# Optimization experiments

Hardware: AMD Instinct MI355X
Metric: run time of the kernel (lower is better)

## Reference

```python
import jax, jax.numpy as jnp
import numpy as np

B, T, D = 4096, 200, 128
K_SHORT = 5


def setup_inputs() -> dict:
    key = jax.random.key(0)
    ks = jax.random.split(key, 8)
    hist_items = jax.random.normal(ks[0], (B, T, D), dtype=jnp.float32)
    hist_mask = jax.random.randint(ks[1], (B, T), 0, 2).astype(bool)
    hist_mask = hist_mask.at[:, 0].set(True)  # avoid fully-masked rows
    hist_age_hours = jax.random.uniform(ks[2], (B, T), dtype=jnp.float32) * 168.0
    hist_popularity = jax.random.uniform(ks[3], (B, T), dtype=jnp.float32)
    s = 1.0 / float(np.sqrt(D))
    Wq = jax.random.normal(ks[4], (D, D), dtype=jnp.float32) * s
    Wk = jax.random.normal(ks[5], (D, D), dtype=jnp.float32) * s
    Wv = jax.random.normal(ks[6], (D, D), dtype=jnp.float32) * s
    gate_w = jax.random.normal(ks[7], (1, 2), dtype=jnp.float32) * 0.5
    gate_b = jnp.zeros((1,), dtype=jnp.float32)
    ln_gamma = jnp.ones((D,), dtype=jnp.float32)
    ln_beta = jnp.zeros((D,), dtype=jnp.float32)
    decay_alpha = jnp.asarray(0.05, dtype=jnp.float32)
    return {"hist_items": hist_items, "hist_mask": hist_mask,
            "hist_age_hours": hist_age_hours, "hist_popularity": hist_popularity,
            "Wq": Wq, "Wk": Wk, "Wv": Wv, "gate_w": gate_w, "gate_b": gate_b,
            "ln_gamma": ln_gamma, "ln_beta": ln_beta, "decay_alpha": decay_alpha}


def reference(hist_items, hist_mask, hist_age_hours, hist_popularity,
              Wq, Wk, Wv, gate_w, gate_b, ln_gamma, ln_beta, decay_alpha):
    dt = hist_items.dtype
    maskf = hist_mask.astype(dt)  # (B,T)
    # learnable time-decay bias
    alpha = jax.nn.softplus(decay_alpha) + 1e-6
    decay = jnp.exp(-alpha * hist_age_hours) * maskf  # (B,T)
    # masked mean of history as the single query
    mean_hist = (hist_items * maskf[..., None]).sum(1) / (maskf.sum(1, keepdims=True) + 1e-6)  # (B,D)
    q = mean_hist @ Wq.T                                # (B,D)
    k = jnp.einsum('btd,ed->bte', hist_items, Wk)       # (B,T,D)
    v = jnp.einsum('btd,ed->bte', hist_items, Wv)       # (B,T,D)
    scale = 1.0 / float(np.sqrt(hist_items.shape[-1]))
    scores = jnp.einsum('bd,btd->bt', q, k) * scale + jnp.log(decay + 1e-12)
    scores = jnp.where(hist_mask, scores, -jnp.inf)
    attn = jax.nn.softmax(scores, axis=-1)              # (B,T)
    long_term = jnp.einsum('bt,btd->bd', attn, v)       # (B,D)
    # vectorized last-K window: positions [cnt-K, cnt)
    cnt = jnp.maximum(hist_mask.sum(1), 1)              # (B,) int
    K = min(K_SHORT, hist_items.shape[1])
    ar = jnp.arange(hist_items.shape[1])[None, :]       # (1,T)
    lastk = (ar >= (cnt[:, None] - K)) & (ar < cnt[:, None])  # (B,T) bool
    lk = lastk.astype(dt)
    denom = jnp.maximum(lk.sum(1, keepdims=True), 1.0)  # (B,1)
    short_term = (hist_items * lk[..., None]).sum(1) / denom  # (B,D)
    mean_pop = (hist_popularity * lk).sum(1) / denom[:, 0]
    mean_rec = (hist_age_hours * lk).sum(1) / denom[:, 0]
    ctx = jnp.stack([mean_pop, mean_rec], axis=-1)      # (B,2)
    g = jax.nn.sigmoid(ctx @ gate_w.T + gate_b)         # (B,1)
    user = g * short_term + (1.0 - g) * long_term       # (B,D)
    # LayerNorm (eps=1e-5, biased variance, matching torch)
    mu = user.mean(-1, keepdims=True)
    var = user.var(-1, keepdims=True)
    return (user - mu) / jnp.sqrt(var + 1e-5) * ln_gamma + ln_beta
```

## Files before the change

kernel.cpp:

```cpp
#include <hip/hip_runtime.h>

#define BB 4096
#define TT 200
#define DD 128
#define KSHORT 5

__device__ __forceinline__ unsigned short f2bf(float x) {
  union { float f; unsigned u; } c; c.f = x;
  unsigned r = c.u + 0x7fffu + ((c.u >> 16) & 1u);
  return (unsigned short)(r >> 16);
}
__device__ __forceinline__ float bf2f(unsigned short h) {
  union { unsigned u; float f; } c; c.u = ((unsigned)h) << 16;
  return c.f;
}

__global__ void detect_mask_kernel(const unsigned* __restrict__ m, int* __restrict__ flag) {
  unsigned bad = 0;
  for (int i = threadIdx.x; i < 1024; i += 64) bad |= (m[i] > 1u) ? 1u : 0u;
  unsigned long long bl = __ballot(bad != 0u);
  if (threadIdx.x == 0) *flag = (bl != 0ULL) ? 1 : 0;
}

__global__ void precompute_A_kernel(const float* __restrict__ Wq,
                                    const float* __restrict__ Wk,
                                    float* __restrict__ A) {
  const int d = blockIdx.x, dp = threadIdx.x;
  float acc = 0.f;
#pragma unroll 8
  for (int e = 0; e < DD; ++e) acc += Wk[e * DD + d] * Wq[e * DD + dp];
  A[d * DD + dp] = acc;
}

__global__ __launch_bounds__(512, 4) void arig_main_kernel(
    const float* __restrict__ items, const void* __restrict__ maskp,
    const float* __restrict__ age, const float* __restrict__ pop,
    const float* __restrict__ Wv, const float* __restrict__ gate_w,
    const float* __restrict__ gate_b, const float* __restrict__ gamma,
    const float* __restrict__ beta, const float* __restrict__ alpha_in,
    const float* __restrict__ A, const int* __restrict__ flagp,
    float* __restrict__ out) {
  __shared__ unsigned short s_items[TT * DD];
  __shared__ float s_mask[TT], s_age[TT], s_pop[TT];
  __shared__ float s_part[8 * DD];
  __shared__ float s_sc[TT], s_attn[TT];
  __shared__ float s_mean[DD], s_short[DD], s_qk[DD], s_wt[DD], s_vec[DD];
  __shared__ float s_scal[8];

  const int b = blockIdx.x;
  const int tid = threadIdx.x;
  const int lane = tid & 63;
  const int w = tid >> 6;
  const int mode = *flagp;

  if (tid < TT) {
    int m;
    if (mode) m = ((const unsigned char*)maskp)[(size_t)b * TT + tid];
    else      m = ((const int*)maskp)[(size_t)b * TT + tid];
    s_mask[tid] = m ? 1.f : 0.f;
    s_age[tid] = age[(size_t)b * TT + tid];
    s_pop[tid] = pop[(size_t)b * TT + tid];
  }
  const float4* gi = (const float4*)(items + (size_t)b * (TT * DD));
  for (int j = tid; j < TT * DD / 4; j += 512) {
    float4 v = gi[j];
    ushort4 h;
    h.x = f2bf(v.x); h.y = f2bf(v.y); h.z = f2bf(v.z); h.w = f2bf(v.w);
    ((ushort4*)s_items)[j] = h;
  }
  __syncthreads();

  if (w == 0) {
    float c = 0.f;
    for (int t = lane; t < TT; t += 64) c += s_mask[t];
#pragma unroll
    for (int o = 32; o > 0; o >>= 1) c += __shfl_xor(c, o);
    if (lane == 0) s_scal[0] = c;
  }
  {
    float a0 = 0.f, a1 = 0.f;
    for (int t = w; t < TT; t += 8) {
      float m = s_mask[t];
      a0 += m * bf2f(s_items[t * DD + lane]);
      a1 += m * bf2f(s_items[t * DD + 64 + lane]);
    }
    s_part[w * DD + lane] = a0;
    s_part[w * DD + 64 + lane] = a1;
  }
  __syncthreads();

  const float cntf = s_scal[0];
  const int cnt = max((int)(cntf + 0.5f), 1);
  const int lo = max(cnt - KSHORT, 0);
  const float dn = (float)(cnt - lo);

  if (tid < DD) {
    float s = 0.f;
#pragma unroll
    for (int k = 0; k < 8; ++k) s += s_part[k * DD + tid];
    s_mean[tid] = s / (cntf + 1e-6f);
    float ss = 0.f;
    for (int t = lo; t < cnt; ++t) ss += bf2f(s_items[t * DD + tid]);
    s_short[tid] = ss / dn;
  }
  if (tid == 0) {
    float sp = 0.f, sr = 0.f;
    for (int t = lo; t < cnt; ++t) { sp += s_pop[t]; sr += s_age[t]; }
    float z = gate_w[0] * (sp / dn) + gate_w[1] * (sr / dn) + gate_b[0];
    s_scal[1] = 1.f / (1.f + expf(-z));
  }
  __syncthreads();

  if (tid < DD) {
    const float4* Ar = (const float4*)(A + tid * DD);
    float acc = 0.f;
#pragma unroll
    for (int j = 0; j < DD / 4; ++j) {
      float4 a4 = Ar[j];
      acc += a4.x * s_mean[4 * j] + a4.y * s_mean[4 * j + 1] +
             a4.z * s_mean[4 * j + 2] + a4.w * s_mean[4 * j + 3];
    }
    s_qk[tid] = acc;
  }
  __syncthreads();

  {
    const float al = log1pf(expf(alpha_in[0])) + 1e-6f;
    const float scale = 0.08838834764831845f;
    const float qk0 = s_qk[lane], qk1 = s_qk[64 + lane];
    for (int t = w; t < TT; t += 8) {
      float p = qk0 * bf2f(s_items[t * DD + lane]) +
                qk1 * bf2f(s_items[t * DD + 64 + lane]);
#pragma unroll
      for (int o = 1; o < 64; o <<= 1) p += __shfl_xor(p, o);
      if (lane == 0) {
        float m = s_mask[t];
        float dec = expf(-al * s_age[t]) * m;
        float sc = p * scale + logf(dec + 1e-12f);
        s_sc[t] = (m > 0.f) ? sc : -INFINITY;
      }
    }
  }
  __syncthreads();

  if (w == 0) {
    float mx = -INFINITY;
    for (int t = lane; t < TT; t += 64) mx = fmaxf(mx, s_sc[t]);
#pragma unroll
    for (int o = 32; o > 0; o >>= 1) mx = fmaxf(mx, __shfl_xor(mx, o));
    float sm = 0.f;
    for (int t = lane; t < TT; t += 64) {
      float e = expf(s_sc[t] - mx);
      s_attn[t] = e;
      sm += e;
    }
#pragma unroll
    for (int o = 32; o > 0; o >>= 1) sm += __shfl_xor(sm, o);
    if (lane == 0) s_scal[2] = sm;
  }
  __syncthreads();

  {
    float a0 = 0.f, a1 = 0.f;
    for (int t = w; t < TT; t += 8) {
      float at = s_attn[t];
      a0 += at * bf2f(s_items[t * DD + lane]);
      a1 += at * bf2f(s_items[t * DD + 64 + lane]);
    }
    s_part[w * DD + lane] = a0;
    s_part[w * DD + 64 + lane] = a1;
  }
  __syncthreads();

  const float inv = 1.f / s_scal[2];
  if (tid < DD) {
    float s = 0.f;
#pragma unroll
    for (int k = 0; k < 8; ++k) s += s_part[k * DD + tid];
    s_wt[tid] = s * inv;
  }
  __syncthreads();

  if (tid < DD) {
    const float4* Wr = (const float4*)(Wv + tid * DD);
    float acc = 0.f;
#pragma unroll
    for (int j = 0; j < DD / 4; ++j) {
      float4 a4 = Wr[j];
      acc += a4.x * s_wt[4 * j] + a4.y * s_wt[4 * j + 1] +
             a4.z * s_wt[4 * j + 2] + a4.w * s_wt[4 * j + 3];
    }
    float g = s_scal[1];
    s_vec[tid] = g * s_short[tid] + (1.f - g) * acc;
  }
  __syncthreads();

  if (w == 0) {
    float x0 = s_vec[lane], x1 = s_vec[64 + lane];
    float s = x0 + x1;
#pragma unroll
    for (int o = 32; o > 0; o >>= 1) s += __shfl_xor(s, o);
    float mu = s * (1.f / 128.f);
    float d0 = x0 - mu, d1 = x1 - mu;
    float s2 = d0 * d0 + d1 * d1;
#pragma unroll
    for (int o = 32; o > 0; o >>= 1) s2 += __shfl_xor(s2, o);
    if (lane == 0) {
      s_scal[3] = mu;
      s_scal[4] = 1.f / sqrtf(s2 * (1.f / 128.f) + 1e-5f);
    }
  }
  __syncthreads();

  if (tid < DD) {
    float y = (s_vec[tid] - s_scal[3]) * s_scal[4] * gamma[tid] + beta[tid];
    out[(size_t)b * DD + tid] = y;
  }
}

extern "C" void kernel_launch(void* const* d_in, const int* in_sizes, int n_in,
                              void* d_out, int out_size, void* d_ws, size_t ws_size,
                              hipStream_t stream) {
  const float* items  = (const float*)d_in[0];
  const void*  maskp  = d_in[1];
  const float* age    = (const float*)d_in[2];
  const float* pop    = (const float*)d_in[3];
  const float* Wq     = (const float*)d_in[4];
  const float* Wk     = (const float*)d_in[5];
  const float* Wv     = (const float*)d_in[6];
  const float* gate_w = (const float*)d_in[7];
  const float* gate_b = (const float*)d_in[8];
  const float* gamma  = (const float*)d_in[9];
  const float* beta   = (const float*)d_in[10];
  const float* alpha  = (const float*)d_in[11];

  int*   flag = (int*)d_ws;
  float* A    = (float*)((char*)d_ws + 256);
  float* outp = (float*)d_out;

  detect_mask_kernel<<<1, 64, 0, stream>>>((const unsigned*)maskp, flag);
  precompute_A_kernel<<<DD, DD, 0, stream>>>(Wq, Wk, A);
  arig_main_kernel<<<BB, 512, 0, stream>>>(items, maskp, age, pop, Wv, gate_w,
                                           gate_b, gamma, beta, alpha, A, flag,
                                           outp);
}
```

Measured before the change: 734.4 us.

## Split into stats and attention kernels with masked-row skipping and online softmax

Replaces the single kernel, which staged all items into LDS as bf16, with two kernels that stream fp32 rows from global memory. Both kernels skip loading rows whose mask is zero, so roughly half the item rows are never read. The first kernel computes the masked mean, short-term window, gate and qk vector. The second runs an online softmax fused with the weighted-V accumulation, and the attention scale is folded into A. The item tensor is read twice (once per kernel, with L2 reuse unlikely at this size), and intermediates now go through workspace.

```diff
diff --git a/kernel.cpp b/kernel.cpp
--- a/kernel.cpp
+++ b/kernel.cpp
@@ -4,16 +4,6 @@
 #define TT 200
 #define DD 128
 #define KSHORT 5
-
-__device__ __forceinline__ unsigned short f2bf(float x) {
-  union { float f; unsigned u; } c; c.f = x;
-  unsigned r = c.u + 0x7fffu + ((c.u >> 16) & 1u);
-  return (unsigned short)(r >> 16);
-}
-__device__ __forceinline__ float bf2f(unsigned short h) {
-  union { unsigned u; float f; } c; c.u = ((unsigned)h) << 16;
-  return c.f;
-}
 
 __global__ void detect_mask_kernel(const unsigned* __restrict__ m, int* __restrict__ flag) {
   unsigned bad = 0;
@@ -29,63 +19,38 @@
   float acc = 0.f;
 #pragma unroll 8
   for (int e = 0; e < DD; ++e) acc += Wk[e * DD + d] * Wq[e * DD + dp];
-  A[d * DD + dp] = acc;
-}
-
-__global__ __launch_bounds__(512, 4) void arig_main_kernel(
+  A[d * DD + dp] = acc * 0.08838834764831845f;
+}
+
+__global__ __launch_bounds__(256, 4) void k1_stats(
     const float* __restrict__ items, const void* __restrict__ maskp,
     const float* __restrict__ age, const float* __restrict__ pop,
-    const float* __restrict__ Wv, const float* __restrict__ gate_w,
-    const float* __restrict__ gate_b, const float* __restrict__ gamma,
-    const float* __restrict__ beta, const float* __restrict__ alpha_in,
+    const float* __restrict__ gate_w, const float* __restrict__ gate_b,
     const float* __restrict__ A, const int* __restrict__ flagp,
-    float* __restrict__ out) {
-  __shared__ unsigned short s_items[TT * DD];
-  __shared__ float s_mask[TT], s_age[TT], s_pop[TT];
-  __shared__ float s_part[8 * DD];
-  __shared__ float s_sc[TT], s_attn[TT];
-  __shared__ float s_mean[DD], s_short[DD], s_qk[DD], s_wt[DD], s_vec[DD];
-  __shared__ float s_scal[8];
-
-  const int b = blockIdx.x;
-  const int tid = threadIdx.x;
-  const int lane = tid & 63;
-  const int w = tid >> 6;
+    float* __restrict__ qkw, float* __restrict__ shortw, float* __restrict__ gw) {
+  __shared__ float s_m[TT];
+  __shared__ float s_pm[8 * DD];
+  __shared__ float s_ps[8 * DD];
+  __shared__ float s_mean[DD];
+  __shared__ float s_scal[4];
+
+  const int b = blockIdx.x, tid = threadIdx.x;
+  const int lane32 = tid & 31, stream = tid >> 5;
   const int mode = *flagp;
 
   if (tid < TT) {
-    int m;
-    if (mode) m = ((const unsigned char*)maskp)[(size_t)b * TT + tid];
-    else      m = ((const int*)maskp)[(size_t)b * TT + tid];
-    s_mask[tid] = m ? 1.f : 0.f;
-    s_age[tid] = age[(size_t)b * TT + tid];
-    s_pop[tid] = pop[(size_t)b * TT + tid];
-  }
-  const float4* gi = (const float4*)(items + (size_t)b * (TT * DD));
-  for (int j = tid; j < TT * DD / 4; j += 512) {
-    float4 v = gi[j];
-    ushort4 h;
-    h.x = f2bf(v.x); h.y = f2bf(v.y); h.z = f2bf(v.z); h.w = f2bf(v.w);
-    ((ushort4*)s_items)[j] = h;
-  }
-  __syncthreads();
-
-  if (w == 0) {
+    int mk = mode ? (int)((const unsigned char*)maskp)[(size_t)b * TT + tid]
+                  : ((const int*)maskp)[(size_t)b * TT + tid];
+    s_m[tid] = mk ? 1.f : 0.f;
+  }
+  __syncthreads();
+
+  if (tid < 64) {
     float c = 0.f;
-    for (int t = lane; t < TT; t += 64) c += s_mask[t];
+    for (int t = tid; t < TT; t += 64) c += s_m[t];
 #pragma unroll
     for (int o = 32; o > 0; o >>= 1) c += __shfl_xor(c, o);
-    if (lane == 0) s_scal[0] = c;
-  }
-  {
-    float a0 = 0.f, a1 = 0.f;
-    for (int t = w; t < TT; t += 8) {
-      float m = s_mask[t];
-      a0 += m * bf2f(s_items[t * DD + lane]);
-      a1 += m * bf2f(s_items[t * DD + 64 + lane]);
-    }
-    s_part[w * DD + lane] = a0;
-    s_part[w * DD + 64 + lane] = a1;
+    if (tid == 0) s_scal[0] = c;
   }
   __syncthreads();
 
@@ -94,20 +59,35 @@
   const int lo = max(cnt - KSHORT, 0);
   const float dn = (float)(cnt - lo);
 
-  if (tid < DD) {
-    float s = 0.f;
-#pragma unroll
-    for (int k = 0; k < 8; ++k) s += s_part[k * DD + tid];
-    s_mean[tid] = s / (cntf + 1e-6f);
-    float ss = 0.f;
-    for (int t = lo; t < cnt; ++t) ss += bf2f(s_items[t * DD + tid]);
-    s_short[tid] = ss / dn;
-  }
-  if (tid == 0) {
+  const float* rowbase = items + (size_t)b * (TT * DD) + lane32 * 4;
+  float4 ms = {0.f, 0.f, 0.f, 0.f}, ss = {0.f, 0.f, 0.f, 0.f};
+  for (int t = stream; t < TT; t += 8) {
+    const float mk = s_m[t];
+    const bool inw = (t >= lo) && (t < cnt);
+    if (mk > 0.f || inw) {
+      float4 v = *(const float4*)(rowbase + t * DD);
+      if (mk > 0.f) { ms.x += v.x; ms.y += v.y; ms.z += v.z; ms.w += v.w; }
+      if (inw)      { ss.x += v.x; ss.y += v.y; ss.z += v.z; ss.w += v.w; }
+    }
+  }
+  *(float4*)&s_pm[stream * DD + lane32 * 4] = ms;
+  *(float4*)&s_ps[stream * DD + lane32 * 4] = ss;
+  __syncthreads();
+
+  if (tid < DD) {
+    float am = 0.f, as = 0.f;
+#pragma unroll
+    for (int s = 0; s < 8; ++s) { am += s_pm[s * DD + tid]; as += s_ps[s * DD + tid]; }
+    s_mean[tid] = am / (cntf + 1e-6f);
+    shortw[(size_t)b * DD + tid] = as / dn;
+  } else if (tid == DD) {
     float sp = 0.f, sr = 0.f;
-    for (int t = lo; t < cnt; ++t) { sp += s_pop[t]; sr += s_age[t]; }
+    for (int t = lo; t < cnt; ++t) {
+      sp += pop[(size_t)b * TT + t];
+      sr += age[(size_t)b * TT + t];
+    }
     float z = gate_w[0] * (sp / dn) + gate_w[1] * (sr / dn) + gate_b[0];
-    s_scal[1] = 1.f / (1.f + expf(-z));
+    gw[b] = 1.f / (1.f + expf(-z));
   }
   __syncthreads();
 
@@ -120,64 +100,79 @@
       acc += a4.x * s_mean[4 * j] + a4.y * s_mean[4 * j + 1] +
              a4.z * s_mean[4 * j + 2] + a4.w * s_mean[4 * j + 3];
     }
-    s_qk[tid] = acc;
-  }
-  __syncthreads();
-
-  {
+    qkw[(size_t)b * DD + tid] = acc;
+  }
+}
+
+__global__ __launch_bounds__(256, 4) void k2_attn(
+    const float* __restrict__ items, const void* __restrict__ maskp,
+    const float* __restrict__ age, const float* __restrict__ Wv,
+    const float* __restrict__ gamma, const float* __restrict__ beta,
+    const float* __restrict__ alpha_in, const int* __restrict__ flagp,
+    const float* __restrict__ qkw, const float* __restrict__ shortw,
+    const float* __restrict__ gw, float* __restrict__ out) {
+  __shared__ float s_bias[TT];
+  __shared__ float s_o[8 * DD];
+  __shared__ float s_ml[16];
+  __shared__ float s_w[DD];
+  __shared__ float s_user[DD];
+  __shared__ float s_scal[4];
+
+  const int b = blockIdx.x, tid = threadIdx.x;
+  const int lane32 = tid & 31, stream = tid >> 5;
+  const int mode = *flagp;
+
+  if (tid < TT) {
+    int mk = mode ? (int)((const unsigned char*)maskp)[(size_t)b * TT + tid]
+                  : ((const int*)maskp)[(size_t)b * TT + tid];
+    const float a = age[(size_t)b * TT + tid];
     const float al = log1pf(expf(alpha_in[0])) + 1e-6f;
-    const float scale = 0.08838834764831845f;
-    const float qk0 = s_qk[lane], qk1 = s_qk[64 + lane];
-    for (int t = w; t < TT; t += 8) {
-      float p = qk0 * bf2f(s_items[t * DD + lane]) +
-                qk1 * bf2f(s_items[t * DD + 64 + lane]);
-#pragma unroll
-      for (int o = 1; o < 64; o <<= 1) p += __shfl_xor(p, o);
-      if (lane == 0) {
-        float m = s_mask[t];
-        float dec = expf(-al * s_age[t]) * m;
-        float sc = p * scale + logf(dec + 1e-12f);
-        s_sc[t] = (m > 0.f) ? sc : -INFINITY;
-      }
-    }
-  }
-  __syncthreads();
-
-  if (w == 0) {
-    float mx = -INFINITY;
-    for (int t = lane; t < TT; t += 64) mx = fmaxf(mx, s_sc[t]);
-#pragma unroll
-    for (int o = 32; o > 0; o >>= 1) mx = fmaxf(mx, __shfl_xor(mx, o));
-    float sm = 0.f;
-    for (int t = lane; t < TT; t += 64) {
-      float e = expf(s_sc[t] - mx);
-      s_attn[t] = e;
-      sm += e;
-    }
-#pragma unroll
-    for (int o = 32; o > 0; o >>= 1) sm += __shfl_xor(sm, o);
-    if (lane == 0) s_scal[2] = sm;
-  }
-  __syncthreads();
-
-  {
-    float a0 = 0.f, a1 = 0.f;
-    for (int t = w; t < TT; t += 8) {
-      float at = s_attn[t];
-      a0 += at * bf2f(s_items[t * DD + lane]);
-      a1 += at * bf2f(s_items[t * DD + 64 + lane]);
-    }
-    s_part[w * DD + lane] = a0;
-    s_part[w * DD + 64 + lane] = a1;
-  }
-  __syncthreads();
-
-  const float inv = 1.f / s_scal[2];
-  if (tid < DD) {
-    float s = 0.f;
-#pragma unroll
-    for (int k = 0; k < 8; ++k) s += s_part[k * DD + tid];
-    s_wt[tid] = s * inv;
+    s_bias[tid] = mk ? logf(expf(-al * a) + 1e-12f) : -1e30f;
+  }
+  __syncthreads();
+
+  const float4 qk = *(const float4*)(qkw + (size_t)b * DD + lane32 * 4);
+  const float* rowbase = items + (size_t)b * (TT * DD) + lane32 * 4;
+
+  float m = -1e30f, l = 0.f;
+  float4 o = {0.f, 0.f, 0.f, 0.f};
+  for (int t = stream; t < TT; t += 8) {
+    const float bb = s_bias[t];
+    if (bb > -1e29f) {
+      float4 v = *(const float4*)(rowbase + t * DD);
+      float p = qk.x * v.x + qk.y * v.y + qk.z * v.z + qk.w * v.w;
+      p += __shfl_xor(p, 1);
+      p += __shfl_xor(p, 2);
+      p += __shfl_xor(p, 4);
+      p += __shfl_xor(p, 8);
+      p += __shfl_xor(p, 16);
+      const float s = p + bb;
+      const float mn = fmaxf(m, s);
+      const float f = __expf(m - mn), e = __expf(s - mn);
+      l = l * f + e;
+      o.x = o.x * f + e * v.x;
+      o.y = o.y * f + e * v.y;
+      o.z = o.z * f + e * v.z;
+      o.w = o.w * f + e * v.w;
+      m = mn;
+    }
+  }
+  *(float4*)&s_o[stream * DD + lane32 * 4] = o;
+  if (lane32 == 0) { s_ml[stream * 2] = m; s_ml[stream * 2 + 1] = l; }
+  __syncthreads();
+
+  if (tid < DD) {
+    float M = s_ml[0];
+#pragma unroll
+    for (int s = 1; s < 8; ++s) M = fmaxf(M, s_ml[2 * s]);
+    float L = 0.f, O = 0.f;
+#pragma unroll
+    for (int s = 0; s < 8; ++s) {
+      const float f = __expf(s_ml[2 * s] - M);
+      L += s_ml[2 * s + 1] * f;
+      O += s_o[s * DD + tid] * f;
+    }
+    s_w[tid] = O / L;
   }
   __syncthreads();
 
@@ -187,34 +182,34 @@
 #pragma unroll
     for (int j = 0; j < DD / 4; ++j) {
       float4 a4 = Wr[j];
-      acc += a4.x * s_wt[4 * j] + a4.y * s_wt[4 * j + 1] +
-             a4.z * s_wt[4 * j + 2] + a4.w * s_wt[4 * j + 3];
-    }
-    float g = s_scal[1];
-    s_vec[tid] = g * s_short[tid] + (1.f - g) * acc;
-  }
-  __syncthreads();
-
-  if (w == 0) {
-    float x0 = s_vec[lane], x1 = s_vec[64 + lane];
-    float s = x0 + x1;
-#pragma unroll
-    for (int o = 32; o > 0; o >>= 1) s += __shfl_xor(s, o);
-    float mu = s * (1.f / 128.f);
-    float d0 = x0 - mu, d1 = x1 - mu;
+      acc += a4.x * s_w[4 * j] + a4.y * s_w[4 * j + 1] +
+             a4.z * s_w[4 * j + 2] + a4.w * s_w[4 * j + 3];
+    }
+    const float g = gw[b];
+    s_user[tid] = g * shortw[(size_t)b * DD + tid] + (1.f - g) * acc;
+  }
+  __syncthreads();
+
+  if (tid < 64) {
+    const float x0 = s_user[tid], x1 = s_user[64 + tid];
+    float su = x0 + x1;
+#pragma unroll
+    for (int off = 32; off > 0; off >>= 1) su += __shfl_xor(su, off);
+    const float mu = su * (1.f / 128.f);
+    const float d0 = x0 - mu, d1 = x1 - mu;
     float s2 = d0 * d0 + d1 * d1;
 #pragma unroll
-    for (int o = 32; o > 0; o >>= 1) s2 += __shfl_xor(s2, o);
-    if (lane == 0) {
-      s_scal[3] = mu;
-      s_scal[4] = 1.f / sqrtf(s2 * (1.f / 128.f) + 1e-5f);
-    }
-  }
-  __syncthreads();
-
-  if (tid < DD) {
-    float y = (s_vec[tid] - s_scal[3]) * s_scal[4] * gamma[tid] + beta[tid];
-    out[(size_t)b * DD + tid] = y;
+    for (int off = 32; off > 0; off >>= 1) s2 += __shfl_xor(s2, off);
+    if (tid == 0) {
+      s_scal[0] = mu;
+      s_scal[1] = 1.f / sqrtf(s2 * (1.f / 128.f) + 1e-5f);
+    }
+  }
+  __syncthreads();
+
+  if (tid < DD) {
+    out[(size_t)b * DD + tid] =
+        (s_user[tid] - s_scal[0]) * s_scal[1] * gamma[tid] + beta[tid];
   }
 }
 
@@ -234,13 +229,18 @@
   const float* beta   = (const float*)d_in[10];
   const float* alpha  = (const float*)d_in[11];
 
-  int*   flag = (int*)d_ws;
-  float* A    = (float*)((char*)d_ws + 256);
-  float* outp = (float*)d_out;
+  char* ws = (char*)d_ws;
+  int*   flag   = (int*)ws;
+  float* A      = (float*)(ws + 256);
+  float* qkw    = (float*)(ws + 256 + 65536);
+  float* shortw = (float*)(ws + 256 + 65536 + 2097152);
+  float* gw     = (float*)(ws + 256 + 65536 + 2 * 2097152);
+  float* outp   = (float*)d_out;
 
   detect_mask_kernel<<<1, 64, 0, stream>>>((const unsigned*)maskp, flag);
   precompute_A_kernel<<<DD, DD, 0, stream>>>(Wq, Wk, A);
-  arig_main_kernel<<<BB, 512, 0, stream>>>(items, maskp, age, pop, Wv, gate_w,
-                                           gate_b, gamma, beta, alpha, A, flag,
-                                           outp);
-}
+  k1_stats<<<BB, 256, 0, stream>>>(items, maskp, age, pop, gate_w, gate_b, A,
+                                   flag, qkw, shortw, gw);
+  k2_attn<<<BB, 256, 0, stream>>>(items, maskp, age, Wv, gamma, beta, alpha,
+                                  flag, qkw, shortw, gw, outp);
+}
```

Measured after the change: 635.6 us. 1.16x faster.
